# Kernel tuning notes

Measured on AMD Instinct MI355X. Metric: run time of the kernel, lower is better.

The kernel has to match this reference:

```python
import jax, jax.numpy as jnp
import numpy as np

K = 15                # top-k codes per token
COMMITMENT_COST = 0.25
N, D, Q = 16384, 256, 8192  # tokens, embed_dim, quant_dim (codebook size)


def setup_inputs() -> dict:
    key = jax.random.key(0)
    k1, k2 = jax.random.split(key)
    z_e = jax.random.normal(k1, (N, D), dtype=jnp.float32)
    # codebook initialized uniform(-1/Q, 1/Q) as in the torch module
    embedding = jax.random.uniform(k2, (Q, D), dtype=jnp.float32,
                                   minval=-1.0 / Q, maxval=1.0 / Q)
    return {"z_e": z_e, "embedding": embedding}


def reference(z_e, embedding):
    # squared L2 distances: [N, Q]
    dist = (jnp.sum(z_e ** 2, axis=1, keepdims=True)
            - 2.0 * (z_e @ embedding.T)
            + jnp.sum(embedding ** 2, axis=1)[None, :])
    # top-k nearest codes (torch.topk(-dist))
    _, top_k_indices = jax.lax.top_k(-dist, K)           # [N, K] int32
    z_q_k = embedding[top_k_indices]                      # [N, K, D] gather
    # k-hot scatter: [N, Q]
    rows = jnp.arange(z_e.shape[0])[:, None]              # [N, 1]
    k_hot = jnp.zeros((z_e.shape[0], embedding.shape[0]), dtype=z_e.dtype)
    k_hot = k_hot.at[rows, top_k_indices].set(1.0)
    z_q = jnp.sum(z_q_k, axis=1)                          # [N, D]
    vq_loss = jnp.mean((z_q - jax.lax.stop_gradient(z_e)) ** 2)
    commitment_loss = jnp.mean((z_e - jax.lax.stop_gradient(z_q)) ** 2)
    total_vq_loss = vq_loss + COMMITMENT_COST * commitment_loss
    # straight-through estimator
    z_q_ste = z_e + jax.lax.stop_gradient(z_q - z_e)
    return (z_q_ste, total_vq_loss, k_hot)
```

## Files before the change

### kernel.cpp

```cpp
#include <hip/hip_runtime.h>


#pragma clang fp contract(off)

#define DIM   256
#define KSEL  15
#define CAP   160
#define NTC   64
#define KR    24

typedef short  s16x8 __attribute__((ext_vector_type(8)));
typedef float  f32x4 __attribute__((ext_vector_type(4)));

__device__ inline unsigned short f2bf(float f) {
  unsigned u = __builtin_bit_cast(unsigned, f);
  unsigned r = (u + 0x7FFFu + ((u >> 16) & 1u)) >> 16;
  return (unsigned short)r;
}

__global__ __launch_bounds__(256)
void prep(const float* __restrict__ emb, unsigned short* __restrict__ ebf,
          float* __restrict__ Enp, int Q) {
  const int gid = blockIdx.x * 256 + threadIdx.x;
  {
    const int i = gid * 8;
    float4 a = *(const float4*)(emb + i);
    float4 b = *(const float4*)(emb + i + 4);
    ushort4 o0; o0.x = f2bf(a.x); o0.y = f2bf(a.y); o0.z = f2bf(a.z); o0.w = f2bf(a.w);
    ushort4 o1; o1.x = f2bf(b.x); o1.y = f2bf(b.y); o1.z = f2bf(b.z); o1.w = f2bf(b.w);
    *(ushort4*)(ebf + i) = o0;
    *(ushort4*)(ebf + i + 4) = o1;
  }
  if (gid < Q) {
    const float* ep = emb + (size_t)gid * DIM;
    float Eh[2];
    for (int h = 0; h < 2; ++h) {
      const int base = 128 * h;
      float r[8];
#pragma unroll
      for (int q2 = 0; q2 < 8; ++q2) { float v = ep[base + q2]; r[q2] = v * v; }
      for (int i = 8; i < 128; i += 8)
#pragma unroll
        for (int q2 = 0; q2 < 8; ++q2) { float v = ep[base + i + q2]; float sq = v * v; r[q2] = r[q2] + sq; }
      Eh[h] = ((r[0] + r[1]) + (r[2] + r[3])) + ((r[4] + r[5]) + (r[6] + r[7]));
    }
    Enp[gid] = Eh[0] + Eh[1];
  }
}

__global__ __launch_bounds__(512, 2)
void vq_capture(const float* __restrict__ z, const unsigned short* __restrict__ ebf,
                int* __restrict__ cntg, unsigned short* __restrict__ candg,
                int N, int Q) {
  __shared__ union {
    unsigned short zbf[NTC][264];
    struct {
      unsigned short candL[NTC][CAP + 2];
      float          scL[NTC][CAP + 1];
    } c;
  } U;
  __shared__ int   cntL[NTC];
  __shared__ float tauL[NTC];
  __shared__ float red[512];

  const int tid  = threadIdx.x;
  const int lane = tid & 63;
  const int wv   = tid >> 6;
  const int t0   = blockIdx.x * NTC;

  {
    const int rt = tid >> 3, rq = tid & 7;
    const float* zp = z + (size_t)(t0 + rt) * DIM;
    float s = 0.f;
#pragma unroll
    for (int m = 0; m < 8; ++m) {
      float4 v = *(const float4*)(zp + 4 * rq + 32 * m);
      s = __builtin_fmaf(v.x, v.x, s);
      s = __builtin_fmaf(v.y, v.y, s);
      s = __builtin_fmaf(v.z, v.z, s);
      s = __builtin_fmaf(v.w, v.w, s);
      ushort4 o; o.x = f2bf(v.x); o.y = f2bf(v.y); o.z = f2bf(v.z); o.w = f2bf(v.w);
      *(ushort4*)&U.zbf[rt][4 * rq + 32 * m] = o;
    }
    red[tid] = s;
  }
  if (tid < NTC) cntL[tid] = 0;
  __syncthreads();

  if (tid < NTC) {
    float s = 0.f;
    for (int j = 0; j < 8; ++j) s += red[tid * 8 + j];
    const float a = 1.0f / (float)Q;
    tauL[tid] = 2.45f * a * 0.57735027f * sqrtf(s) - 1e-6f;
  }

  s16x8 afrag[4][8];
  {
    const int arow = lane & 15;
    const int kq   = (lane >> 4) * 8;
#pragma unroll
    for (int tt = 0; tt < 4; ++tt) {
#pragma unroll
      for (int ks = 0; ks < 8; ++ks)
        afrag[tt][ks] = *(const s16x8*)&U.zbf[tt * 16 + arow][ks * 32 + kq];
    }
  }
  __syncthreads();

  {
    const int ncw  = Q / 8;
    const int c0w  = wv * ncw;
    const int col  = lane & 15;
    const int kq8  = (lane >> 4) * 8;
    const int rbase = (lane >> 4) * 4;
    const unsigned short* bbase = ebf + ((size_t)(c0w + col) * DIM + kq8);

    uint4 buf0[8], buf1[8];
#pragma unroll
    for (int ks = 0; ks < 8; ++ks) buf0[ks] = *(const uint4*)(bbase + ks * 32);

    for (int it = 0; it < 64; it += 2) {
      {
        const unsigned short* bp = bbase + (size_t)(it + 1) * 16 * DIM;
#pragma unroll
        for (int ks = 0; ks < 8; ++ks) buf1[ks] = *(const uint4*)(bp + ks * 32);
      }
      {
        f32x4 acc0 = {0.f, 0.f, 0.f, 0.f};
        f32x4 acc1 = {0.f, 0.f, 0.f, 0.f};
        f32x4 acc2 = {0.f, 0.f, 0.f, 0.f};
        f32x4 acc3 = {0.f, 0.f, 0.f, 0.f};
#pragma unroll
        for (int ks = 0; ks < 8; ++ks) {
          s16x8 bfv = __builtin_bit_cast(s16x8, buf0[ks]);
          acc0 = __builtin_amdgcn_mfma_f32_16x16x32_bf16(afrag[0][ks], bfv, acc0, 0, 0, 0);
          acc1 = __builtin_amdgcn_mfma_f32_16x16x32_bf16(afrag[1][ks], bfv, acc1, 0, 0, 0);
          acc2 = __builtin_amdgcn_mfma_f32_16x16x32_bf16(afrag[2][ks], bfv, acc2, 0, 0, 0);
          acc3 = __builtin_amdgcn_mfma_f32_16x16x32_bf16(afrag[3][ks], bfv, acc3, 0, 0, 0);
        }
        const int code = c0w + it * 16 + col;
#pragma unroll
        for (int r = 0; r < 4; ++r) {
          const int tk0 = rbase + r;
          if (acc0[r] > tauL[tk0]) {
            int s = atomicAdd(&cntL[tk0], 1);
            if (s < CAP) { U.c.candL[tk0][s] = (unsigned short)code; U.c.scL[tk0][s] = acc0[r]; }
          }
          const int tk1 = 16 + rbase + r;
          if (acc1[r] > tauL[tk1]) {
            int s = atomicAdd(&cntL[tk1], 1);
            if (s < CAP) { U.c.candL[tk1][s] = (unsigned short)code; U.c.scL[tk1][s] = acc1[r]; }
          }
          const int tk2 = 32 + rbase + r;
          if (acc2[r] > tauL[tk2]) {
            int s = atomicAdd(&cntL[tk2], 1);
            if (s < CAP) { U.c.candL[tk2][s] = (unsigned short)code; U.c.scL[tk2][s] = acc2[r]; }
          }
          const int tk3 = 48 + rbase + r;
          if (acc3[r] > tauL[tk3]) {
            int s = atomicAdd(&cntL[tk3], 1);
            if (s < CAP) { U.c.candL[tk3][s] = (unsigned short)code; U.c.scL[tk3][s] = acc3[r]; }
          }
        }
      }
      if (it + 2 < 64) {
        const unsigned short* bp = bbase + (size_t)(it + 2) * 16 * DIM;
#pragma unroll
        for (int ks = 0; ks < 8; ++ks) buf0[ks] = *(const uint4*)(bp + ks * 32);
      }
      {
        f32x4 acc0 = {0.f, 0.f, 0.f, 0.f};
        f32x4 acc1 = {0.f, 0.f, 0.f, 0.f};
        f32x4 acc2 = {0.f, 0.f, 0.f, 0.f};
        f32x4 acc3 = {0.f, 0.f, 0.f, 0.f};
#pragma unroll
        for (int ks = 0; ks < 8; ++ks) {
          s16x8 bfv = __builtin_bit_cast(s16x8, buf1[ks]);
          acc0 = __builtin_amdgcn_mfma_f32_16x16x32_bf16(afrag[0][ks], bfv, acc0, 0, 0, 0);
          acc1 = __builtin_amdgcn_mfma_f32_16x16x32_bf16(afrag[1][ks], bfv, acc1, 0, 0, 0);
          acc2 = __builtin_amdgcn_mfma_f32_16x16x32_bf16(afrag[2][ks], bfv, acc2, 0, 0, 0);
          acc3 = __builtin_amdgcn_mfma_f32_16x16x32_bf16(afrag[3][ks], bfv, acc3, 0, 0, 0);
        }
        const int code = c0w + (it + 1) * 16 + col;
#pragma unroll
        for (int r = 0; r < 4; ++r) {
          const int tk0 = rbase + r;
          if (acc0[r] > tauL[tk0]) {
            int s = atomicAdd(&cntL[tk0], 1);
            if (s < CAP) { U.c.candL[tk0][s] = (unsigned short)code; U.c.scL[tk0][s] = acc0[r]; }
          }
          const int tk1 = 16 + rbase + r;
          if (acc1[r] > tauL[tk1]) {
            int s = atomicAdd(&cntL[tk1], 1);
            if (s < CAP) { U.c.candL[tk1][s] = (unsigned short)code; U.c.scL[tk1][s] = acc1[r]; }
          }
          const int tk2 = 32 + rbase + r;
          if (acc2[r] > tauL[tk2]) {
            int s = atomicAdd(&cntL[tk2], 1);
            if (s < CAP) { U.c.candL[tk2][s] = (unsigned short)code; U.c.scL[tk2][s] = acc2[r]; }
          }
          const int tk3 = 48 + rbase + r;
          if (acc3[r] > tauL[tk3]) {
            int s = atomicAdd(&cntL[tk3], 1);
            if (s < CAP) { U.c.candL[tk3][s] = (unsigned short)code; U.c.scL[tk3][s] = acc3[r]; }
          }
        }
      }
    }
  }
  __syncthreads();

  if ((tid & 7) == 0) {
    const int t = tid >> 3;
    const int m = min(cntL[t], CAP);
    const int keep = min(m, KR);
    for (int k = 0; k < keep; ++k) {
      float bv = -3.4e38f; int bj = 0;
      for (int j = 0; j < m; ++j) {
        float v = U.c.scL[t][j];
        if (v > bv) { bv = v; bj = j; }
      }
      U.c.scL[t][bj] = -3.5e38f;
      candg[(size_t)(t0 + t) * KR + k] = U.c.candL[t][bj];
    }
    cntg[t0 + t] = keep;
  }
}

__global__ __launch_bounds__(256, 4)
void vq_out(const float* __restrict__ z, const float* __restrict__ emb,
            const float* __restrict__ Enp, const int* __restrict__ cntg,
            const unsigned short* __restrict__ candg, float* __restrict__ out,
            int N, int Q) {
  __shared__ __align__(16) float zld[4][DIM + 4];
  __shared__ float red[256];

  const int tid  = threadIdx.x;
  const int lane = tid & 63;
  const int wv   = tid >> 6;
  const int gw   = blockIdx.x * 4 + wv;
  float* khot = out + (size_t)N * DIM + 1;

  float lpacc = 0.f;

  for (int ti = 0; ti < 4; ++ti) {
    const int t = gw * 4 + ti;

    {
      const float4 v = *(const float4*)(z + (size_t)t * DIM + 4 * lane);
      *(float4*)&zld[wv][4 * lane] = v;
    }
    const int mb = min(cntg[t], KR);
    const int c_mine = (lane < mb) ? (int)candg[(size_t)t * KR + lane] : 0;

    __builtin_amdgcn_s_waitcnt(0);

    float Arow;
    {
      float Aval = 0.f;
      if (lane == 0) {
        const float* zl = &zld[wv][0];
        float Ah[2];
        for (int h = 0; h < 2; ++h) {
          const int base = 128 * h;
          float r[8];
#pragma unroll
          for (int q2 = 0; q2 < 8; ++q2) { float v = zl[base + q2]; r[q2] = v * v; }
          for (int i = 8; i < 128; i += 8)
#pragma unroll
            for (int q2 = 0; q2 < 8; ++q2) { float v = zl[base + i + q2]; float sq = v * v; r[q2] = r[q2] + sq; }
          Ah[h] = ((r[0] + r[1]) + (r[2] + r[3])) + ((r[4] + r[5]) + (r[6] + r[7]));
        }
        Aval = Ah[0] + Ah[1];
      }
      Arow = __shfl(Aval, 0);
    }

    float scv = 3.4e38f;
    if (lane < mb) {
      const float* el = emb + (size_t)c_mine * DIM;
      const float* zl = &zld[wv][0];
      float bch = 0.f;
      for (int i = 0; i < 256; i += 8) {
        float4 ea = *(const float4*)(el + i);
        float4 eb = *(const float4*)(el + i + 4);
        float4 za = *(const float4*)(zl + i);
        float4 zb = *(const float4*)(zl + i + 4);
        bch = __builtin_fmaf(za.x, ea.x, bch);
        bch = __builtin_fmaf(za.y, ea.y, bch);
        bch = __builtin_fmaf(za.z, ea.z, bch);
        bch = __builtin_fmaf(za.w, ea.w, bch);
        bch = __builtin_fmaf(zb.x, eb.x, bch);
        bch = __builtin_fmaf(zb.y, eb.y, bch);
        bch = __builtin_fmaf(zb.z, eb.z, bch);
        bch = __builtin_fmaf(zb.w, eb.w, bch);
      }
      scv = (Arow - 2.0f * bch) + Enp[c_mine];
    }

    int mywin = 0;
    {
      unsigned okey = __builtin_bit_cast(unsigned, scv);
      okey = (okey & 0x80000000u) ? ~okey : (okey | 0x80000000u);
      unsigned long long key = (lane < mb)
          ? (((unsigned long long)okey << 32) | (unsigned)c_mine)
          : 0xFFFFFFFFFFFFFFFFull;
      for (int k = 0; k < KSEL; ++k) {
        unsigned long long m = key;
#pragma unroll
        for (int d = 1; d < 64; d <<= 1) {
          unsigned long long o = __shfl_xor(m, d);
          m = (o < m) ? o : m;
        }
        int wcode = ((unsigned)(m >> 32) == 0xFFFFFFFFu) ? 0 : (int)(unsigned)(m & 0xFFFFFFFFull);
        if (lane == k) mywin = wcode;
        if (key == m) key = 0xFFFFFFFFFFFFFFFFull;
      }
    }

    {
      float* rowp = khot + (size_t)t * Q;
      if (lane < 3) rowp[lane] = 0.f;
      if (lane == 3) rowp[Q - 1] = 0.f;
      float4* p4 = (float4*)(rowp + 3);
      const f32x4 zv = {0.f, 0.f, 0.f, 0.f};
#pragma unroll
      for (int i = 0; i < 32; ++i) {
        const int idx = lane + 64 * i;
        if (idx < 2047) *(f32x4*)&p4[idx] = zv;
      }
    }
    asm volatile("s_waitcnt vmcnt(0)" ::: "memory");
    if (lane < KSEL) khot[(size_t)t * Q + mywin] = 1.0f;

    {
      float4 zq4 = make_float4(0.f, 0.f, 0.f, 0.f);
      for (int k = 0; k < KSEL; ++k) {
        const int c = __shfl(mywin, k);
        const float4 e4 = *(const float4*)(emb + (size_t)c * DIM + 4 * lane);
        zq4.x = zq4.x + e4.x; zq4.y = zq4.y + e4.y;
        zq4.z = zq4.z + e4.z; zq4.w = zq4.w + e4.w;
      }
      const float4 zv = *(const float4*)&zld[wv][4 * lane];
      float d0 = zq4.x - zv.x, d1 = zq4.y - zv.y, d2 = zq4.z - zv.z, d3 = zq4.w - zv.w;
      float4 o; o.x = zv.x + d0; o.y = zv.y + d1; o.z = zv.z + d2; o.w = zv.w + d3;
      *(float4*)(out + (size_t)t * DIM + 4 * lane) = o;
      lpacc = __builtin_fmaf(d0, d0, lpacc);
      lpacc = __builtin_fmaf(d1, d1, lpacc);
      lpacc = __builtin_fmaf(d2, d2, lpacc);
      lpacc = __builtin_fmaf(d3, d3, lpacc);
    }
    __builtin_amdgcn_s_waitcnt(0);
  }

  red[tid] = lpacc;
  __syncthreads();
  for (int s = 128; s > 0; s >>= 1) {
    if (tid < s) red[tid] += red[tid + s];
    __syncthreads();
  }
  if (tid == 0) {
    const float scale = 1.25f / (float)((size_t)N * DIM);
    atomicAdd(out + (size_t)N * DIM, red[0] * scale);
  }
}

extern "C" void kernel_launch(void* const* d_in, const int* in_sizes, int n_in,
                              void* d_out, int out_size, void* d_ws, size_t ws_size,
                              hipStream_t stream) {
  const float* z   = (const float*)d_in[0];
  const float* emb = (const float*)d_in[1];
  float* out = (float*)d_out;
  const int N = in_sizes[0] / DIM;
  const int Q = in_sizes[1] / DIM;

  unsigned short* ebf = (unsigned short*)d_ws;
  char* p = (char*)d_ws + (size_t)Q * DIM * 2;
  float* Enp  = (float*)p;           p += (size_t)Q * 4;
  int*   cntg = (int*)p;             p += (size_t)N * 4;
  unsigned short* candg = (unsigned short*)p;

  hipMemsetAsync((char*)d_out + (size_t)N * DIM * sizeof(float), 0, sizeof(float), stream);
  prep<<<dim3((Q * DIM) / (8 * 256)), dim3(256), 0, stream>>>(emb, ebf, Enp, Q);
  vq_capture<<<dim3(N / NTC), dim3(512), 0, stream>>>(z, ebf, cntg, candg, N, Q);
  vq_out<<<dim3(N / (4 * 4)), dim3(256), 0, stream>>>(z, emb, Enp, cntg, candg, out, N, Q);
}
```

Measured before the change: 901.8 us.

## Fuse candidate capture and output kernels into one mega kernel

Merges the capture and output kernels so each block rescoring its own 64 tokens reads candidates from shared memory instead of a global candidate buffer, removing a kernel launch and the global round trip. The wave-shuffle top-15 selection is replaced by a serial lane-0 scan over shared scores, and k-hot zero fills use nontemporal stores. The output phase now runs inside the capture block's occupancy limits (512 threads, 2 blocks/CU) with a larger shared union, and the serial selection may lengthen per-token latency.

```diff
diff --git a/kernel.cpp b/kernel.cpp
--- a/kernel.cpp
+++ b/kernel.cpp
@@ -49,16 +49,23 @@
 }
 
 __global__ __launch_bounds__(512, 2)
-void vq_capture(const float* __restrict__ z, const unsigned short* __restrict__ ebf,
-                int* __restrict__ cntg, unsigned short* __restrict__ candg,
-                int N, int Q) {
-  __shared__ union {
+void vq_mega(const float* __restrict__ z, const float* __restrict__ emb,
+             const unsigned short* __restrict__ ebf, const float* __restrict__ Enp,
+             float* __restrict__ out, int N, int Q) {
+  __shared__ __align__(16) union {
     unsigned short zbf[NTC][264];
     struct {
       unsigned short candL[NTC][CAP + 2];
       float          scL[NTC][CAP + 1];
     } c;
+    struct {
+      float zrow[8][DIM + 4];
+      float scw[8][28];
+      int   winw[8][16];
+    } o;
   } U;
+  __shared__ unsigned short candT[NTC][KR];
+  __shared__ int   cntT[NTC];
   __shared__ int   cntL[NTC];
   __shared__ float tauL[NTC];
   __shared__ float red[512];
@@ -67,6 +74,7 @@
   const int lane = tid & 63;
   const int wv   = tid >> 6;
   const int t0   = blockIdx.x * NTC;
+  float* khot = out + (size_t)N * DIM + 1;
 
   {
     const int rt = tid >> 3, rq = tid & 7;
@@ -221,45 +229,30 @@
         if (v > bv) { bv = v; bj = j; }
       }
       U.c.scL[t][bj] = -3.5e38f;
-      candg[(size_t)(t0 + t) * KR + k] = U.c.candL[t][bj];
-    }
-    cntg[t0 + t] = keep;
-  }
-}
-
-__global__ __launch_bounds__(256, 4)
-void vq_out(const float* __restrict__ z, const float* __restrict__ emb,
-            const float* __restrict__ Enp, const int* __restrict__ cntg,
-            const unsigned short* __restrict__ candg, float* __restrict__ out,
-            int N, int Q) {
-  __shared__ __align__(16) float zld[4][DIM + 4];
-  __shared__ float red[256];
-
-  const int tid  = threadIdx.x;
-  const int lane = tid & 63;
-  const int wv   = tid >> 6;
-  const int gw   = blockIdx.x * 4 + wv;
-  float* khot = out + (size_t)N * DIM + 1;
+      candT[t][k] = U.c.candL[t][bj];
+    }
+    cntT[t] = keep;
+  }
+  __syncthreads();
 
   float lpacc = 0.f;
-
-  for (int ti = 0; ti < 4; ++ti) {
-    const int t = gw * 4 + ti;
+  for (int ti = 0; ti < 8; ++ti) {
+    const int tl = wv * 8 + ti;
+    const int t  = t0 + tl;
 
     {
       const float4 v = *(const float4*)(z + (size_t)t * DIM + 4 * lane);
-      *(float4*)&zld[wv][4 * lane] = v;
-    }
-    const int mb = min(cntg[t], KR);
-    const int c_mine = (lane < mb) ? (int)candg[(size_t)t * KR + lane] : 0;
-
+      *(float4*)&U.o.zrow[wv][4 * lane] = v;
+    }
+    const int mb = cntT[tl];
+    const int cm = (lane < mb) ? (int)candT[tl][lane] : 0;
     __builtin_amdgcn_s_waitcnt(0);
 
     float Arow;
     {
       float Aval = 0.f;
       if (lane == 0) {
-        const float* zl = &zld[wv][0];
+        const float* zl = &U.o.zrow[wv][0];
         float Ah[2];
         for (int h = 0; h < 2; ++h) {
           const int base = 128 * h;
@@ -278,8 +271,8 @@
 
     float scv = 3.4e38f;
     if (lane < mb) {
-      const float* el = emb + (size_t)c_mine * DIM;
-      const float* zl = &zld[wv][0];
+      const float* el = emb + (size_t)cm * DIM;
+      const float* zl = &U.o.zrow[wv][0];
       float bch = 0.f;
       for (int i = 0; i < 256; i += 8) {
         float4 ea = *(const float4*)(el + i);
@@ -295,53 +288,48 @@
         bch = __builtin_fmaf(zb.z, eb.z, bch);
         bch = __builtin_fmaf(zb.w, eb.w, bch);
       }
-      scv = (Arow - 2.0f * bch) + Enp[c_mine];
-    }
-
-    int mywin = 0;
-    {
-      unsigned okey = __builtin_bit_cast(unsigned, scv);
-      okey = (okey & 0x80000000u) ? ~okey : (okey | 0x80000000u);
-      unsigned long long key = (lane < mb)
-          ? (((unsigned long long)okey << 32) | (unsigned)c_mine)
-          : 0xFFFFFFFFFFFFFFFFull;
+      scv = (Arow - 2.0f * bch) + Enp[cm];
+    }
+    if (lane < KR) U.o.scw[wv][lane] = (lane < mb) ? scv : 3.4e38f;
+    __builtin_amdgcn_s_waitcnt(0);
+
+    if (lane == 0) {
       for (int k = 0; k < KSEL; ++k) {
-        unsigned long long m = key;
-#pragma unroll
-        for (int d = 1; d < 64; d <<= 1) {
-          unsigned long long o = __shfl_xor(m, d);
-          m = (o < m) ? o : m;
-        }
-        int wcode = ((unsigned)(m >> 32) == 0xFFFFFFFFu) ? 0 : (int)(unsigned)(m & 0xFFFFFFFFull);
-        if (lane == k) mywin = wcode;
-        if (key == m) key = 0xFFFFFFFFFFFFFFFFull;
-      }
-    }
+        float bv = 3.4e38f; int bc = 0x7fffffff; int bj = -1;
+        for (int j = 0; j < mb; ++j) {
+          float v = U.o.scw[wv][j]; int c = candT[tl][j];
+          if (v < bv || (v == bv && c < bc)) { bv = v; bc = c; bj = j; }
+        }
+        if (bj >= 0) U.o.scw[wv][bj] = 3.5e38f;
+        U.o.winw[wv][k] = (bj >= 0) ? bc : 0;
+      }
+    }
+    __builtin_amdgcn_s_waitcnt(0);
 
     {
       float* rowp = khot + (size_t)t * Q;
       if (lane < 3) rowp[lane] = 0.f;
       if (lane == 3) rowp[Q - 1] = 0.f;
       float4* p4 = (float4*)(rowp + 3);
-      const f32x4 zv = {0.f, 0.f, 0.f, 0.f};
+      const f32x4 zv4 = {0.f, 0.f, 0.f, 0.f};
 #pragma unroll
       for (int i = 0; i < 32; ++i) {
         const int idx = lane + 64 * i;
-        if (idx < 2047) *(f32x4*)&p4[idx] = zv;
-      }
-    }
-    asm volatile("s_waitcnt vmcnt(0)" ::: "memory");
-    if (lane < KSEL) khot[(size_t)t * Q + mywin] = 1.0f;
+        if (idx < 2047) __builtin_nontemporal_store(zv4, (f32x4*)&p4[idx]);
+      }
+      asm volatile("s_waitcnt vmcnt(0)" ::: "memory");
+      if (lane < KSEL) rowp[U.o.winw[wv][lane]] = 1.0f;
+    }
 
     {
       float4 zq4 = make_float4(0.f, 0.f, 0.f, 0.f);
       for (int k = 0; k < KSEL; ++k) {
-        const int c = __shfl(mywin, k);
+        const int c = U.o.winw[wv][k];
         const float4 e4 = *(const float4*)(emb + (size_t)c * DIM + 4 * lane);
         zq4.x = zq4.x + e4.x; zq4.y = zq4.y + e4.y;
         zq4.z = zq4.z + e4.z; zq4.w = zq4.w + e4.w;
       }
-      const float4 zv = *(const float4*)&zld[wv][4 * lane];
+      const float4 zv = *(const float4*)&U.o.zrow[wv][4 * lane];
       float d0 = zq4.x - zv.x, d1 = zq4.y - zv.y, d2 = zq4.z - zv.z, d3 = zq4.w - zv.w;
       float4 o; o.x = zv.x + d0; o.y = zv.y + d1; o.z = zv.z + d2; o.w = zv.w + d3;
       *(float4*)(out + (size_t)t * DIM + 4 * lane) = o;
@@ -355,7 +343,7 @@
 
   red[tid] = lpacc;
   __syncthreads();
-  for (int s = 128; s > 0; s >>= 1) {
+  for (int s = 256; s > 0; s >>= 1) {
     if (tid < s) red[tid] += red[tid + s];
     __syncthreads();
   }
@@ -376,12 +364,9 @@
 
   unsigned short* ebf = (unsigned short*)d_ws;
   char* p = (char*)d_ws + (size_t)Q * DIM * 2;
-  float* Enp  = (float*)p;           p += (size_t)Q * 4;
-  int*   cntg = (int*)p;             p += (size_t)N * 4;
-  unsigned short* candg = (unsigned short*)p;
+  float* Enp  = (float*)p;
 
   hipMemsetAsync((char*)d_out + (size_t)N * DIM * sizeof(float), 0, sizeof(float), stream);
   prep<<<dim3((Q * DIM) / (8 * 256)), dim3(256), 0, stream>>>(emb, ebf, Enp, Q);
-  vq_capture<<<dim3(N / NTC), dim3(512), 0, stream>>>(z, ebf, cntg, candg, N, Q);
-  vq_out<<<dim3(N / (4 * 4)), dim3(256), 0, stream>>>(z, emb, Enp, cntg, candg, out, N, Q);
+  vq_mega<<<dim3(N / NTC), dim3(512), 0, stream>>>(z, emb, ebf, Enp, out, N, Q);
 }
```

Result: slower. 1.060 ms (+17.5%).

## Aggregate candidate appends with ballot and write k-hot rows in one pass

Applied to the files above, without the earlier changes.

In the capture kernel, per-lane LDS atomics for candidate appends are replaced by a wave ballot, so each 16-lane group issues one atomicAdd per token row and lanes derive their slots from popcount ranks. In the output kernel, the k-hot row is written in a single nontemporal pass that places the ones inline, instead of zero-fill, wait, then scatter. The explicit vmcnt waits are dropped, and each wave now handles 2 tokens instead of 4, doubling the grid. This targets LDS atomic contention and the store serialization in the output stage, at the cost of extra ballot, shuffle and compare work per tile.

```diff
diff --git a/kernel.cpp b/kernel.cpp
--- a/kernel.cpp
+++ b/kernel.cpp
@@ -47,6 +47,28 @@
     Enp[gid] = Eh[0] + Eh[1];
   }
 }
+
+#define BAPPEND(ACC, TKOFF, CODE) do {                                        \
+    _Pragma("unroll")                                                         \
+    for (int r = 0; r < 4; ++r) {                                             \
+      const int tk = (TKOFF) + rbase + r;                                     \
+      const bool pr = (ACC)[r] > tauL[tk];                                    \
+      const unsigned long long bm = __ballot(pr);                             \
+      const unsigned gm = (unsigned)((bm >> (grp << 4)) & 0xFFFFull);         \
+      if (gm) {                                                               \
+        const int ldr  = __builtin_ctz(gm);                                   \
+        const int rank = __popc(gm & ((1u << sub) - 1u));                     \
+        int base = 0;                                                         \
+        if (sub == ldr) base = atomicAdd(&cntL[tk], __popc(gm));              \
+        base = __shfl(base, (grp << 4) + ldr);                                \
+        if (pr) {                                                             \
+          const int s = base + rank;                                          \
+          if (s < CAP) { U.c.candL[tk][s] = (unsigned short)(CODE);           \
+                         U.c.scL[tk][s] = (ACC)[r]; }                         \
+        }                                                                     \
+      }                                                                       \
+    }                                                                         \
+  } while (0)
 
 __global__ __launch_bounds__(512, 2)
 void vq_capture(const float* __restrict__ z, const unsigned short* __restrict__ ebf,
@@ -66,6 +88,8 @@
   const int tid  = threadIdx.x;
   const int lane = tid & 63;
   const int wv   = tid >> 6;
+  const int grp  = lane >> 4;
+  const int sub  = lane & 15;
   const int t0   = blockIdx.x * NTC;
 
   {
@@ -96,8 +120,8 @@
 
   s16x8 afrag[4][8];
   {
-    const int arow = lane & 15;
-    const int kq   = (lane >> 4) * 8;
+    const int arow = sub;
+    const int kq   = grp * 8;
 #pragma unroll
     for (int tt = 0; tt < 4; ++tt) {
 #pragma unroll
@@ -110,9 +134,9 @@
   {
     const int ncw  = Q / 8;
     const int c0w  = wv * ncw;
-    const int col  = lane & 15;
-    const int kq8  = (lane >> 4) * 8;
-    const int rbase = (lane >> 4) * 4;
+    const int col  = sub;
+    const int kq8  = grp * 8;
+    const int rbase = grp * 4;
     const unsigned short* bbase = ebf + ((size_t)(c0w + col) * DIM + kq8);
 
     uint4 buf0[8], buf1[8];
@@ -139,29 +163,10 @@
           acc3 = __builtin_amdgcn_mfma_f32_16x16x32_bf16(afrag[3][ks], bfv, acc3, 0, 0, 0);
         }
         const int code = c0w + it * 16 + col;
-#pragma unroll
-        for (int r = 0; r < 4; ++r) {
-          const int tk0 = rbase + r;
-          if (acc0[r] > tauL[tk0]) {
-            int s = atomicAdd(&cntL[tk0], 1);
-            if (s < CAP) { U.c.candL[tk0][s] = (unsigned short)code; U.c.scL[tk0][s] = acc0[r]; }
-          }
-          const int tk1 = 16 + rbase + r;
-          if (acc1[r] > tauL[tk1]) {
-            int s = atomicAdd(&cntL[tk1], 1);
-            if (s < CAP) { U.c.candL[tk1][s] = (unsigned short)code; U.c.scL[tk1][s] = acc1[r]; }
-          }
-          const int tk2 = 32 + rbase + r;
-          if (acc2[r] > tauL[tk2]) {
-            int s = atomicAdd(&cntL[tk2], 1);
-            if (s < CAP) { U.c.candL[tk2][s] = (unsigned short)code; U.c.scL[tk2][s] = acc2[r]; }
-          }
-          const int tk3 = 48 + rbase + r;
-          if (acc3[r] > tauL[tk3]) {
-            int s = atomicAdd(&cntL[tk3], 1);
-            if (s < CAP) { U.c.candL[tk3][s] = (unsigned short)code; U.c.scL[tk3][s] = acc3[r]; }
-          }
-        }
+        BAPPEND(acc0,  0, code);
+        BAPPEND(acc1, 16, code);
+        BAPPEND(acc2, 32, code);
+        BAPPEND(acc3, 48, code);
       }
       if (it + 2 < 64) {
         const unsigned short* bp = bbase + (size_t)(it + 2) * 16 * DIM;
@@ -182,29 +187,10 @@
           acc3 = __builtin_amdgcn_mfma_f32_16x16x32_bf16(afrag[3][ks], bfv, acc3, 0, 0, 0);
         }
         const int code = c0w + (it + 1) * 16 + col;
-#pragma unroll
-        for (int r = 0; r < 4; ++r) {
-          const int tk0 = rbase + r;
-          if (acc0[r] > tauL[tk0]) {
-            int s = atomicAdd(&cntL[tk0], 1);
-            if (s < CAP) { U.c.candL[tk0][s] = (unsigned short)code; U.c.scL[tk0][s] = acc0[r]; }
-          }
-          const int tk1 = 16 + rbase + r;
-          if (acc1[r] > tauL[tk1]) {
-            int s = atomicAdd(&cntL[tk1], 1);
-            if (s < CAP) { U.c.candL[tk1][s] = (unsigned short)code; U.c.scL[tk1][s] = acc1[r]; }
-          }
-          const int tk2 = 32 + rbase + r;
-          if (acc2[r] > tauL[tk2]) {
-            int s = atomicAdd(&cntL[tk2], 1);
-            if (s < CAP) { U.c.candL[tk2][s] = (unsigned short)code; U.c.scL[tk2][s] = acc2[r]; }
-          }
-          const int tk3 = 48 + rbase + r;
-          if (acc3[r] > tauL[tk3]) {
-            int s = atomicAdd(&cntL[tk3], 1);
-            if (s < CAP) { U.c.candL[tk3][s] = (unsigned short)code; U.c.scL[tk3][s] = acc3[r]; }
-          }
-        }
+        BAPPEND(acc0,  0, code);
+        BAPPEND(acc1, 16, code);
+        BAPPEND(acc2, 32, code);
+        BAPPEND(acc3, 48, code);
       }
     }
   }
@@ -243,8 +229,8 @@
 
   float lpacc = 0.f;
 
-  for (int ti = 0; ti < 4; ++ti) {
-    const int t = gw * 4 + ti;
+  for (int ti = 0; ti < 2; ++ti) {
+    const int t = gw * 2 + ti;
 
     {
       const float4 v = *(const float4*)(z + (size_t)t * DIM + 4 * lane);
@@ -318,26 +304,54 @@
       }
     }
 
+    int w[KSEL];
+#pragma unroll
+    for (int k = 0; k < KSEL; ++k) w[k] = __shfl(mywin, k);
+
     {
       float* rowp = khot + (size_t)t * Q;
-      if (lane < 3) rowp[lane] = 0.f;
-      if (lane == 3) rowp[Q - 1] = 0.f;
+      if (lane < 4) {
+        const int tgt = (lane < 3) ? lane : (Q - 1);
+        float hv = 0.f;
+#pragma unroll
+        for (int k = 0; k < KSEL; ++k) hv = (w[k] == tgt) ? 1.f : hv;
+        rowp[tgt] = hv;
+      }
+      unsigned pm = 0;
+#pragma unroll
+      for (int k = 0; k < KSEL; ++k) {
+        const int wl = w[k] - 3;
+        if (wl >= 0 && w[k] < Q - 1) {
+          const int idx4 = wl >> 2;
+          if ((idx4 & 63) == lane) pm |= 1u << (idx4 >> 6);
+        }
+      }
       float4* p4 = (float4*)(rowp + 3);
-      const f32x4 zv = {0.f, 0.f, 0.f, 0.f};
 #pragma unroll
       for (int i = 0; i < 32; ++i) {
         const int idx = lane + 64 * i;
-        if (idx < 2047) *(f32x4*)&p4[idx] = zv;
-      }
-    }
-    asm volatile("s_waitcnt vmcnt(0)" ::: "memory");
-    if (lane < KSEL) khot[(size_t)t * Q + mywin] = 1.0f;
+        if (idx < 2047) {
+          f32x4 v = {0.f, 0.f, 0.f, 0.f};
+          if ((pm >> i) & 1u) {
+            const int bf = 3 + 4 * idx;
+#pragma unroll
+            for (int k = 0; k < KSEL; ++k) {
+              const int d = w[k] - bf;
+              v.x = (d == 0) ? 1.f : v.x;
+              v.y = (d == 1) ? 1.f : v.y;
+              v.z = (d == 2) ? 1.f : v.z;
+              v.w = (d == 3) ? 1.f : v.w;
+            }
+          }
+          __builtin_nontemporal_store(v, (f32x4*)&p4[idx]);
+        }
+      }
+    }
 
     {
       float4 zq4 = make_float4(0.f, 0.f, 0.f, 0.f);
       for (int k = 0; k < KSEL; ++k) {
-        const int c = __shfl(mywin, k);
-        const float4 e4 = *(const float4*)(emb + (size_t)c * DIM + 4 * lane);
+        const float4 e4 = *(const float4*)(emb + (size_t)w[k] * DIM + 4 * lane);
         zq4.x = zq4.x + e4.x; zq4.y = zq4.y + e4.y;
         zq4.z = zq4.z + e4.z; zq4.w = zq4.w + e4.w;
       }
@@ -350,7 +364,6 @@
       lpacc = __builtin_fmaf(d2, d2, lpacc);
       lpacc = __builtin_fmaf(d3, d3, lpacc);
     }
-    __builtin_amdgcn_s_waitcnt(0);
   }
 
   red[tid] = lpacc;
@@ -383,5 +396,5 @@
   hipMemsetAsync((char*)d_out + (size_t)N * DIM * sizeof(float), 0, sizeof(float), stream);
   prep<<<dim3((Q * DIM) / (8 * 256)), dim3(256), 0, stream>>>(emb, ebf, Enp, Q);
   vq_capture<<<dim3(N / NTC), dim3(512), 0, stream>>>(z, ebf, cntg, candg, N, Q);
-  vq_out<<<dim3(N / (4 * 4)), dim3(256), 0, stream>>>(z, emb, Enp, cntg, candg, out, N, Q);
+  vq_out<<<dim3(N / 8), dim3(256), 0, stream>>>(z, emb, Enp, cntg, candg, out, N, Q);
 }
```

Result: slower. 933.5 us (+3.5%).

## Split codebook scan across two blocks per 32-token tile and merge candidates

Applied to the files above, without the earlier changes.

The capture kernel now uses 256-thread blocks handling 32 tokens. Each token tile gets two blocks, and each block scans half of the codebook, with a launch bound of four blocks per CU instead of two. Each half writes its own candidate list, and the output kernel merges the two lists (up to 48 candidates) before exact rescoring. The aim is higher occupancy and fewer registers per thread. The cost is twice the codebook reads per token, the loss of the explicit double-buffered B loads, and more candidates to rescore in the output kernel.

```diff
diff --git a/kernel.cpp b/kernel.cpp
--- a/kernel.cpp
+++ b/kernel.cpp
@@ -5,8 +5,8 @@
 
 #define DIM   256
 #define KSEL  15
-#define CAP   160
-#define NTC   64
+#define NTC2  32
+#define CAP2  112
 #define KR    24
 
 typedef short  s16x8 __attribute__((ext_vector_type(8)));
@@ -48,25 +48,29 @@
   }
 }
 
-__global__ __launch_bounds__(512, 2)
+__global__ __launch_bounds__(256, 4)
 void vq_capture(const float* __restrict__ z, const unsigned short* __restrict__ ebf,
                 int* __restrict__ cntg, unsigned short* __restrict__ candg,
                 int N, int Q) {
   __shared__ union {
-    unsigned short zbf[NTC][264];
+    unsigned short zbf[NTC2][264];
     struct {
-      unsigned short candL[NTC][CAP + 2];
-      float          scL[NTC][CAP + 1];
+      unsigned short candL[NTC2][CAP2 + 2];
+      float          scL[NTC2][CAP2 + 1];
     } c;
   } U;
-  __shared__ int   cntL[NTC];
-  __shared__ float tauL[NTC];
-  __shared__ float red[512];
+  __shared__ int   cntL[NTC2];
+  __shared__ float tauL[NTC2];
+  __shared__ float red[256];
 
   const int tid  = threadIdx.x;
   const int lane = tid & 63;
   const int wv   = tid >> 6;
-  const int t0   = blockIdx.x * NTC;
+  const int grp  = lane >> 4;
+  const int sub  = lane & 15;
+  const int tb   = blockIdx.x >> 1;
+  const int half = blockIdx.x & 1;
+  const int t0   = tb * NTC2;
 
   {
     const int rt = tid >> 3, rq = tid & 7;
@@ -84,22 +88,22 @@
     }
     red[tid] = s;
   }
-  if (tid < NTC) cntL[tid] = 0;
+  if (tid < NTC2) cntL[tid] = 0;
   __syncthreads();
 
-  if (tid < NTC) {
+  if (tid < NTC2) {
     float s = 0.f;
     for (int j = 0; j < 8; ++j) s += red[tid * 8 + j];
     const float a = 1.0f / (float)Q;
     tauL[tid] = 2.45f * a * 0.57735027f * sqrtf(s) - 1e-6f;
   }
 
-  s16x8 afrag[4][8];
+  s16x8 afrag[2][8];
   {
-    const int arow = lane & 15;
-    const int kq   = (lane >> 4) * 8;
-#pragma unroll
-    for (int tt = 0; tt < 4; ++tt) {
+    const int arow = sub;
+    const int kq   = grp * 8;
+#pragma unroll
+    for (int tt = 0; tt < 2; ++tt) {
 #pragma unroll
       for (int ks = 0; ks < 8; ++ks)
         afrag[tt][ks] = *(const s16x8*)&U.zbf[tt * 16 + arow][ks * 32 + kq];
@@ -108,102 +112,39 @@
   __syncthreads();
 
   {
-    const int ncw  = Q / 8;
-    const int c0w  = wv * ncw;
-    const int col  = lane & 15;
-    const int kq8  = (lane >> 4) * 8;
-    const int rbase = (lane >> 4) * 4;
+    const int c0w  = half * (Q >> 1) + wv * 1024;
+    const int col  = sub;
+    const int kq8  = grp * 8;
+    const int rbase = grp * 4;
     const unsigned short* bbase = ebf + ((size_t)(c0w + col) * DIM + kq8);
 
-    uint4 buf0[8], buf1[8];
-#pragma unroll
-    for (int ks = 0; ks < 8; ++ks) buf0[ks] = *(const uint4*)(bbase + ks * 32);
-
-    for (int it = 0; it < 64; it += 2) {
+    for (int it = 0; it < 64; ++it) {
+      uint4 buf[8];
       {
-        const unsigned short* bp = bbase + (size_t)(it + 1) * 16 * DIM;
-#pragma unroll
-        for (int ks = 0; ks < 8; ++ks) buf1[ks] = *(const uint4*)(bp + ks * 32);
-      }
-      {
-        f32x4 acc0 = {0.f, 0.f, 0.f, 0.f};
-        f32x4 acc1 = {0.f, 0.f, 0.f, 0.f};
-        f32x4 acc2 = {0.f, 0.f, 0.f, 0.f};
-        f32x4 acc3 = {0.f, 0.f, 0.f, 0.f};
-#pragma unroll
-        for (int ks = 0; ks < 8; ++ks) {
-          s16x8 bfv = __builtin_bit_cast(s16x8, buf0[ks]);
-          acc0 = __builtin_amdgcn_mfma_f32_16x16x32_bf16(afrag[0][ks], bfv, acc0, 0, 0, 0);
-          acc1 = __builtin_amdgcn_mfma_f32_16x16x32_bf16(afrag[1][ks], bfv, acc1, 0, 0, 0);
-          acc2 = __builtin_amdgcn_mfma_f32_16x16x32_bf16(afrag[2][ks], bfv, acc2, 0, 0, 0);
-          acc3 = __builtin_amdgcn_mfma_f32_16x16x32_bf16(afrag[3][ks], bfv, acc3, 0, 0, 0);
+        const unsigned short* bp = bbase + (size_t)it * 16 * DIM;
+#pragma unroll
+        for (int ks = 0; ks < 8; ++ks) buf[ks] = *(const uint4*)(bp + ks * 32);
+      }
+      f32x4 acc0 = {0.f, 0.f, 0.f, 0.f};
+      f32x4 acc1 = {0.f, 0.f, 0.f, 0.f};
+#pragma unroll
+      for (int ks = 0; ks < 8; ++ks) {
+        s16x8 bfv = __builtin_bit_cast(s16x8, buf[ks]);
+        acc0 = __builtin_amdgcn_mfma_f32_16x16x32_bf16(afrag[0][ks], bfv, acc0, 0, 0, 0);
+        acc1 = __builtin_amdgcn_mfma_f32_16x16x32_bf16(afrag[1][ks], bfv, acc1, 0, 0, 0);
+      }
+      const int code = c0w + it * 16 + col;
+#pragma unroll
+      for (int r = 0; r < 4; ++r) {
+        const int tk0 = rbase + r;
+        if (acc0[r] > tauL[tk0]) {
+          int s = atomicAdd(&cntL[tk0], 1);
+          if (s < CAP2) { U.c.candL[tk0][s] = (unsigned short)code; U.c.scL[tk0][s] = acc0[r]; }
         }
-        const int code = c0w + it * 16 + col;
-#pragma unroll
-        for (int r = 0; r < 4; ++r) {
-          const int tk0 = rbase + r;
-          if (acc0[r] > tauL[tk0]) {
-            int s = atomicAdd(&cntL[tk0], 1);
-            if (s < CAP) { U.c.candL[tk0][s] = (unsigned short)code; U.c.scL[tk0][s] = acc0[r]; }
-          }
-          const int tk1 = 16 + rbase + r;
-          if (acc1[r] > tauL[tk1]) {
-            int s = atomicAdd(&cntL[tk1], 1);
-            if (s < CAP) { U.c.candL[tk1][s] = (unsigned short)code; U.c.scL[tk1][s] = acc1[r]; }
-          }
-          const int tk2 = 32 + rbase + r;
-          if (acc2[r] > tauL[tk2]) {
-            int s = atomicAdd(&cntL[tk2], 1);
-            if (s < CAP) { U.c.candL[tk2][s] = (unsigned short)code; U.c.scL[tk2][s] = acc2[r]; }
-          }
-          const int tk3 = 48 + rbase + r;
-          if (acc3[r] > tauL[tk3]) {
-            int s = atomicAdd(&cntL[tk3], 1);
-            if (s < CAP) { U.c.candL[tk3][s] = (unsigned short)code; U.c.scL[tk3][s] = acc3[r]; }
-          }
-        }
-      }
-      if (it + 2 < 64) {
-        const unsigned short* bp = bbase + (size_t)(it + 2) * 16 * DIM;
-#pragma unroll
-        for (int ks = 0; ks < 8; ++ks) buf0[ks] = *(const uint4*)(bp + ks * 32);
-      }
-      {
-        f32x4 acc0 = {0.f, 0.f, 0.f, 0.f};
-        f32x4 acc1 = {0.f, 0.f, 0.f, 0.f};
-        f32x4 acc2 = {0.f, 0.f, 0.f, 0.f};
-        f32x4 acc3 = {0.f, 0.f, 0.f, 0.f};
-#pragma unroll
-        for (int ks = 0; ks < 8; ++ks) {
-          s16x8 bfv = __builtin_bit_cast(s16x8, buf1[ks]);
-          acc0 = __builtin_amdgcn_mfma_f32_16x16x32_bf16(afrag[0][ks], bfv, acc0, 0, 0, 0);
-          acc1 = __builtin_amdgcn_mfma_f32_16x16x32_bf16(afrag[1][ks], bfv, acc1, 0, 0, 0);
-          acc2 = __builtin_amdgcn_mfma_f32_16x16x32_bf16(afrag[2][ks], bfv, acc2, 0, 0, 0);
-          acc3 = __builtin_amdgcn_mfma_f32_16x16x32_bf16(afrag[3][ks], bfv, acc3, 0, 0, 0);
-        }
-        const int code = c0w + (it + 1) * 16 + col;
-#pragma unroll
-        for (int r = 0; r < 4; ++r) {
-          const int tk0 = rbase + r;
-          if (acc0[r] > tauL[tk0]) {
-            int s = atomicAdd(&cntL[tk0], 1);
-            if (s < CAP) { U.c.candL[tk0][s] = (unsigned short)code; U.c.scL[tk0][s] = acc0[r]; }
-          }
-          const int tk1 = 16 + rbase + r;
-          if (acc1[r] > tauL[tk1]) {
-            int s = atomicAdd(&cntL[tk1], 1);
-            if (s < CAP) { U.c.candL[tk1][s] = (unsigned short)code; U.c.scL[tk1][s] = acc1[r]; }
-          }
-          const int tk2 = 32 + rbase + r;
-          if (acc2[r] > tauL[tk2]) {
-            int s = atomicAdd(&cntL[tk2], 1);
-            if (s < CAP) { U.c.candL[tk2][s] = (unsigned short)code; U.c.scL[tk2][s] = acc2[r]; }
-          }
-          const int tk3 = 48 + rbase + r;
-          if (acc3[r] > tauL[tk3]) {
-            int s = atomicAdd(&cntL[tk3], 1);
-            if (s < CAP) { U.c.candL[tk3][s] = (unsigned short)code; U.c.scL[tk3][s] = acc3[r]; }
-          }
+        const int tk1 = 16 + rbase + r;
+        if (acc1[r] > tauL[tk1]) {
+          int s = atomicAdd(&cntL[tk1], 1);
+          if (s < CAP2) { U.c.candL[tk1][s] = (unsigned short)code; U.c.scL[tk1][s] = acc1[r]; }
         }
       }
     }
@@ -212,8 +153,9 @@
 
   if ((tid & 7) == 0) {
     const int t = tid >> 3;
-    const int m = min(cntL[t], CAP);
+    const int m = min(cntL[t], CAP2);
     const int keep = min(m, KR);
+    unsigned short* cg = candg + ((size_t)(t0 + t) * 2 + half) * KR;
     for (int k = 0; k < keep; ++k) {
       float bv = -3.4e38f; int bj = 0;
       for (int j = 0; j < m; ++j) {
@@ -221,9 +163,9 @@
         if (v > bv) { bv = v; bj = j; }
       }
       U.c.scL[t][bj] = -3.5e38f;
-      candg[(size_t)(t0 + t) * KR + k] = U.c.candL[t][bj];
-    }
-    cntg[t0 + t] = keep;
+      cg[k] = U.c.candL[t][bj];
+    }
+    cntg[(t0 + t) * 2 + half] = keep;
   }
 }
 
@@ -250,8 +192,14 @@
       const float4 v = *(const float4*)(z + (size_t)t * DIM + 4 * lane);
       *(float4*)&zld[wv][4 * lane] = v;
     }
-    const int mb = min(cntg[t], KR);
-    const int c_mine = (lane < mb) ? (int)candg[(size_t)t * KR + lane] : 0;
+    const int m0 = min(cntg[2 * t], KR);
+    const int m1 = min(cntg[2 * t + 1], KR);
+    const int mb = m0 + m1;
+    int c_mine = 0;
+    if (lane < mb) {
+      const unsigned short* cg = candg + (size_t)t * 2 * KR;
+      c_mine = (lane < m0) ? (int)cg[lane] : (int)cg[KR + (lane - m0)];
+    }
 
     __builtin_amdgcn_s_waitcnt(0);
 
@@ -377,11 +325,11 @@
   unsigned short* ebf = (unsigned short*)d_ws;
   char* p = (char*)d_ws + (size_t)Q * DIM * 2;
   float* Enp  = (float*)p;           p += (size_t)Q * 4;
-  int*   cntg = (int*)p;             p += (size_t)N * 4;
+  int*   cntg = (int*)p;             p += (size_t)N * 2 * 4;
   unsigned short* candg = (unsigned short*)p;
 
   hipMemsetAsync((char*)d_out + (size_t)N * DIM * sizeof(float), 0, sizeof(float), stream);
   prep<<<dim3((Q * DIM) / (8 * 256)), dim3(256), 0, stream>>>(emb, ebf, Enp, Q);
-  vq_capture<<<dim3(N / NTC), dim3(512), 0, stream>>>(z, ebf, cntg, candg, N, Q);
-  vq_out<<<dim3(N / (4 * 4)), dim3(256), 0, stream>>>(z, emb, Enp, cntg, candg, out, N, Q);
-}
+  vq_capture<<<dim3((N / NTC2) * 2), dim3(256), 0, stream>>>(z, ebf, cntg, candg, N, Q);
+  vq_out<<<dim3(N / 16), dim3(256), 0, stream>>>(z, emb, Enp, cntg, candg, out, N, Q);
+}
```

Result: slower. 990.8 us (+9.9%).
